# Kernel tuning notes

Measured on AMD Instinct MI355X. Metric: run time of the kernel, lower is better.

## Reference

```python
import jax, jax.numpy as jnp
import numpy as np

N_NODES = 100_000
NODES_PER_GRAPH = 100
NUM_GRAPHS = N_NODES // NODES_PER_GRAPH
N_EDGES = 1_600_000
NUM_FEATURES = 32
NUM_CLASSES = 10
K_POOL = 30          # DGCNN sort-pool k
OUT_LEN = 16
IN_LEN = 97          # 32+32+32+1 concatenated GCN features
NUM_ITER = 3


def setup_inputs() -> dict:
    key = jax.random.key(0)
    ks = jax.random.split(key, 12)
    x = jax.random.normal(ks[0], (N_NODES, NUM_FEATURES), dtype=jnp.float32)
    # edges constrained within each graph: gid*npg + local index
    gid = (jnp.arange(N_EDGES) % NUM_GRAPHS).astype(jnp.int64)
    src_loc = jax.random.randint(ks[1], (N_EDGES,), 0, NODES_PER_GRAPH)
    dst_loc = jax.random.randint(ks[2], (N_EDGES,), 0, NODES_PER_GRAPH)
    edge_src = gid * NODES_PER_GRAPH + src_loc
    edge_dst = gid * NODES_PER_GRAPH + dst_loc
    batch = jnp.arange(N_NODES, dtype=jnp.int64) // NODES_PER_GRAPH
    s = 1.0 / np.sqrt(NUM_FEATURES)
    params = dict(
        W1=jax.random.normal(ks[3], (NUM_FEATURES, 32), jnp.float32) * s,
        b1=jnp.zeros((32,), jnp.float32),
        W2=jax.random.normal(ks[4], (32, 32), jnp.float32) * (1/np.sqrt(32)),
        b2=jnp.zeros((32,), jnp.float32),
        W3=jax.random.normal(ks[5], (32, 32), jnp.float32) * (1/np.sqrt(32)),
        b3=jnp.zeros((32,), jnp.float32),
        W4=jax.random.normal(ks[6], (32, 1), jnp.float32) * (1/np.sqrt(32)),
        b4=jnp.zeros((1,), jnp.float32),
        Wcap=jax.random.normal(ks[7], (NUM_CLASSES, OUT_LEN, IN_LEN), jnp.float32) * (1/np.sqrt(IN_LEN)),
    )
    return dict(x=x, edge_src=edge_src, edge_dst=edge_dst, batch=batch, **params)


def gcn_conv(x, W, b, edge_src, edge_dst, dinv):
    # PyG GCNConv: h = xW, out[d] = sum_e dinv[s]*dinv[d]*h[s] (incl. self loops), + b
    h = x @ W
    msg = h[edge_src] * (dinv[edge_src] * dinv[edge_dst])[:, None]
    out = jax.ops.segment_sum(msg, edge_dst, num_segments=x.shape[0])
    out = out + h * (dinv * dinv)[:, None]  # self-loop term
    return out + b


def reference(x, edge_src, edge_dst, batch, W1, b1, W2, b2, W3, b3, W4, b4, Wcap):
    n = x.shape[0]
    # symmetric normalization with self loops (degree over incoming edges + 1)
    deg = jnp.zeros((n,), x.dtype).at[edge_dst].add(1.0) + 1.0
    dinv = jax.lax.rsqrt(deg)

    x1 = jnp.tanh(gcn_conv(x,  W1, b1, edge_src, edge_dst, dinv))
    x2 = jnp.tanh(gcn_conv(x1, W2, b2, edge_src, edge_dst, dinv))
    x3 = jnp.tanh(gcn_conv(x2, W3, b3, edge_src, edge_dst, dinv))
    x4 = jnp.tanh(gcn_conv(x3, W4, b4, edge_src, edge_dst, dinv))
    feat = jnp.concatenate([x1, x2, x3, x4], axis=-1)  # [N, 97]

    # global_sort_pool: per-graph descending sort on last channel, keep top-k nodes
    B = n // NODES_PER_GRAPH
    fg = feat.reshape(B, NODES_PER_GRAPH, IN_LEN)
    order = jnp.argsort(-fg[..., -1], axis=1)[:, :K_POOL]            # [B, k]
    pooled = jnp.take_along_axis(fg, order[..., None], axis=1)        # [B, k, 97]

    # CapsuleLinear, shared weight, k-means routing, Tanimoto similarity
    priors = jnp.einsum('bil,cel->bice', pooled, Wcap)                # [B, k, C, 16]
    pr_sq = jnp.sum(priors * priors, axis=-1)                         # [B, k, C]
    out = jnp.mean(priors, axis=1, keepdims=True)                     # [B, 1, C, 16]
    for _ in range(NUM_ITER):
        xy = jnp.sum(priors * out, axis=-1)                           # [B, k, C]
        out_sq = jnp.sum(out * out, axis=-1)                          # [B, 1, C]
        sim = xy / (pr_sq + out_sq - xy)                              # Tanimoto
        probs = jax.nn.softmax(sim, axis=1)[..., None]                # over in_capsules
        out = jnp.sum(probs * priors, axis=1, keepdims=True)
    out = out[:, 0]                                                   # [B, C, 16]
    classes = jnp.linalg.norm(out, axis=-1)                           # [B, C]
    return classes
```

## Files before the change

### kernel.cpp

```cpp
#include <hip/hip_runtime.h>
#include <math.h>

#define NGRAPH 1000
#define NPG    100
#define EPG    1600
#define NF     32
#define NC     10
#define KP     30
#define OUTL   16
#define INL    97
#define NITER  3

#define NTV    512
#define NTF    1024

#define XSTR   36
#define FSTR   100
#define HSTR   36
#define PSTR   164
#define CSRMAX 1920
#define ZROW   (NPG * XSTR)

#define WS_EDGES_BYTES ((size_t)NGRAPH * EPG * 4)
#define WCAPB_UINT4    2560
#define WS_V10_BYTES   (WS_EDGES_BYTES + (size_t)WCAPB_UINT4 * 16)

#define PIDX(i, c) ((i) * PSTR + (c) * OUTL)

typedef __attribute__((ext_vector_type(8))) short bf16x8;
typedef __attribute__((ext_vector_type(4))) float f32x4;

__device__ __forceinline__ float4 ld4(const float* p) { return *reinterpret_cast<const float4*>(p); }
__device__ __forceinline__ void st4(float* p, float4 v) { *reinterpret_cast<float4*>(p) = v; }
__device__ __forceinline__ float dot4(float4 a, float4 b) { return a.x*b.x + a.y*b.y + a.z*b.z + a.w*b.w; }
__device__ __forceinline__ float tanh_fast(float x) {
  float e = __expf(2.f * x);
  return 1.f - 2.f / (e + 1.f);
}
__device__ __forceinline__ unsigned f2bf(float f) {
  unsigned u = __float_as_uint(f);
  u += 0x7FFFu + ((u >> 16) & 1u);
  return u >> 16;
}

__global__ void prek_edges(const int* __restrict__ esrc, const int* __restrict__ edst,
                           unsigned int* __restrict__ wsE) {
  __shared__ unsigned int t[64][65];
  const int kb = blockIdx.x % (EPG / 64);
  const int gb = blockIdx.x / (EPG / 64);
  const int lane = threadIdx.x & 63;
  const int row  = threadIdx.x >> 6;
  #pragma unroll
  for (int r = row; r < 64; r += 4) {
    int k = kb * 64 + r;
    int g = gb * 64 + lane;
    if (g < NGRAPH) {
      int idx = k * NGRAPH + g;
      int si = esrc[idx] - g * NPG;
      int di = edst[idx] - g * NPG;
      t[r][lane] = (unsigned int)((si << 8) | di);
    }
  }
  __syncthreads();
  #pragma unroll
  for (int r = row; r < 64; r += 4) {
    int g = gb * 64 + r;
    int k = kb * 64 + lane;
    if (g < NGRAPH) wsE[(size_t)g * EPG + k] = t[lane][r];
  }
}

__global__ void prek_capB(const float* __restrict__ Wcap, uint4* __restrict__ wcapB) {
  int o = blockIdx.x * 256 + threadIdx.x;
  if (o >= WCAPB_UINT4) return;
  int ks  = o / 640;
  int rem = o - ks * 640;
  int n   = rem >> 6;
  int ln  = rem & 63;
  int e   = ln & 15;
  int k0  = ks * 32 + ((ln >> 4) << 3);
  const float* wr = Wcap + (n * OUTL + e) * INL;
  unsigned v[8];
  #pragma unroll
  for (int j = 0; j < 8; ++j) {
    int k = k0 + j;
    v[j] = f2bf((k < INL) ? wr[k] : 0.f);
  }
  uint4 pk;
  pk.x = v[0] | (v[1] << 16); pk.y = v[2] | (v[3] << 16);
  pk.z = v[4] | (v[5] << 16); pk.w = v[6] | (v[7] << 16);
  wcapB[o] = pk;
}

struct SMemV13 {
  float feat[NPG * FSTR];
  union {
    struct {
      float hs[(NPG + 1) * XSTR];
      float W[NF * NF];
      float bias2[2][NF];
      unsigned short csr16[CSRMAX];
      int cnt[NPG];
      float dinv[NPG];
      int ptr[NPG + 1];
    } a;
    struct {
      float priors[KP * PSTR];
      float prsq[KP * NC];
      float simbuf[KP * NC];
      float outv[NC * OUTL];
      uint4 pooledB[512];
    } b;
  } u;
  int order[KP];
};

__global__ __launch_bounds__(NTV, 4) void gcn_caps_v13(
    const float* __restrict__ x,
    const unsigned int* __restrict__ wsE,
    const float* __restrict__ W1, const float* __restrict__ b1,
    const float* __restrict__ W2, const float* __restrict__ b2,
    const float* __restrict__ W3, const float* __restrict__ b3,
    const float* __restrict__ W4, const float* __restrict__ b4,
    const uint4* __restrict__ wcapB,
    float* __restrict__ out)
{
  extern __shared__ char smraw[];
  SMemV13& s = *reinterpret_cast<SMemV13*>(smraw);
  const int g = blockIdx.x;
  const int tid = threadIdx.x;

  if (tid < NPG) s.u.a.cnt[tid] = 0;
  if (tid >= 128 && tid < 128 + XSTR) s.u.a.hs[ZROW + (tid - 128)] = 0.f;
  for (int i = tid; i < NF * NF; i += NTV) s.u.a.W[i] = W1[i];
  if (tid < NF) s.u.a.bias2[0][tid] = b1[tid];
  __syncthreads();

  const unsigned int* eg = wsE + (size_t)g * EPG;
  for (int k = tid; k < EPG; k += NTV) atomicAdd(&s.u.a.cnt[eg[k] & 0xFF], 1);
  __syncthreads();

  if (tid < 64) {
    int j = tid;
    int n0 = 2 * j, n1 = 2 * j + 1;
    int r0 = (n0 < NPG) ? s.u.a.cnt[n0] : 0;
    int r1 = (n1 < NPG) ? s.u.a.cnt[n1] : 0;
    int q0 = (r0 + 3) & ~3, q1 = (r1 + 3) & ~3;
    int t = q0 + q1;
    int run = t;
    #pragma unroll
    for (int off = 1; off < 64; off <<= 1) {
      int u = __shfl_up(run, off);
      if (j >= off) run += u;
    }
    int excl = run - t;
    if (n0 < NPG) {
      s.u.a.ptr[n0] = excl;
      s.u.a.dinv[n0] = rsqrtf((float)r0 + 1.0f);
      s.u.a.cnt[n0] = excl;
      for (int k = excl + r0; k < excl + q0; ++k) s.u.a.csr16[k] = (unsigned short)ZROW;
    }
    if (n1 < NPG) {
      int e1 = excl + q0;
      s.u.a.ptr[n1] = e1;
      s.u.a.dinv[n1] = rsqrtf((float)r1 + 1.0f);
      s.u.a.cnt[n1] = e1;
      for (int k = e1 + r1; k < e1 + q1; ++k) s.u.a.csr16[k] = (unsigned short)ZROW;
    }
    if (j == 63) s.u.a.ptr[NPG] = run;
  }
  __syncthreads();

  for (int k = tid; k < EPG; k += NTV) {
    unsigned int p = eg[k];
    int pos = atomicAdd(&s.u.a.cnt[p & 0xFF], 1);
    s.u.a.csr16[pos] = (unsigned short)(((p >> 8) & 0xFF) * XSTR);
  }
  __syncthreads();

  const float4* xr = reinterpret_cast<const float4*>(x + (size_t)g * NPG * NF);

  for (int l = 0; l < 3; ++l) {
    if (tid < 25 * 8) {
      int nd = tid >> 3, cq = tid & 7;
      float4 ac0 = make_float4(0,0,0,0), ac1 = ac0, ac2 = ac0, ac3 = ac0;
      #pragma unroll
      for (int kq = 0; kq < 8; ++kq) {
        float4 a0, a1, a2, a3;
        if (l == 0) {
          a0 = xr[(nd     ) * 8 + kq]; a1 = xr[(nd + 25) * 8 + kq];
          a2 = xr[(nd + 50) * 8 + kq]; a3 = xr[(nd + 75) * 8 + kq];
        } else {
          int cb = (l - 1) * NF + kq * 4;
          a0 = ld4(&s.feat[(nd     ) * FSTR + cb]);
          a1 = ld4(&s.feat[(nd + 25) * FSTR + cb]);
          a2 = ld4(&s.feat[(nd + 50) * FSTR + cb]);
          a3 = ld4(&s.feat[(nd + 75) * FSTR + cb]);
        }
        const float v0[4] = {a0.x, a0.y, a0.z, a0.w};
        const float v1[4] = {a1.x, a1.y, a1.z, a1.w};
        const float v2[4] = {a2.x, a2.y, a2.z, a2.w};
        const float v3[4] = {a3.x, a3.y, a3.z, a3.w};
        #pragma unroll
        for (int j = 0; j < 4; ++j) {
          float4 w4 = ld4(&s.u.a.W[(kq * 4 + j) * NF + cq * 4]);
          ac0.x += v0[j]*w4.x; ac0.y += v0[j]*w4.y; ac0.z += v0[j]*w4.z; ac0.w += v0[j]*w4.w;
          ac1.x += v1[j]*w4.x; ac1.y += v1[j]*w4.y; ac1.z += v1[j]*w4.z; ac1.w += v1[j]*w4.w;
          ac2.x += v2[j]*w4.x; ac2.y += v2[j]*w4.y; ac2.z += v2[j]*w4.z; ac2.w += v2[j]*w4.w;
          ac3.x += v3[j]*w4.x; ac3.y += v3[j]*w4.y; ac3.z += v3[j]*w4.z; ac3.w += v3[j]*w4.w;
        }
      }
      float d0 = s.u.a.dinv[nd], d1 = s.u.a.dinv[nd + 25];
      float d2 = s.u.a.dinv[nd + 50], d3 = s.u.a.dinv[nd + 75];
      ac0.x*=d0; ac0.y*=d0; ac0.z*=d0; ac0.w*=d0;
      ac1.x*=d1; ac1.y*=d1; ac1.z*=d1; ac1.w*=d1;
      ac2.x*=d2; ac2.y*=d2; ac2.z*=d2; ac2.w*=d2;
      ac3.x*=d3; ac3.y*=d3; ac3.z*=d3; ac3.w*=d3;
      st4(&s.u.a.hs[(nd     ) * XSTR + cq * 4], ac0);
      st4(&s.u.a.hs[(nd + 25) * XSTR + cq * 4], ac1);
      st4(&s.u.a.hs[(nd + 50) * XSTR + cq * 4], ac2);
      st4(&s.u.a.hs[(nd + 75) * XSTR + cq * 4], ac3);
    }
    __syncthreads();

    if (l == 0) {
      for (int i = tid; i < NF * NF; i += NTV) s.u.a.W[i] = W2[i];
      if (tid < NF) s.u.a.bias2[1][tid] = b2[tid];
    } else if (l == 1) {
      for (int i = tid; i < NF * NF; i += NTV) s.u.a.W[i] = W3[i];
      if (tid < NF) s.u.a.bias2[0][tid] = b3[tid];
    } else {
      if (tid < NF) s.u.a.W[tid] = W4[tid];
      if (tid == NTV - 1) s.u.a.bias2[1][0] = b4[0];
    }

    for (int o = tid; o < NPG * 16; o += NTV) {
      int d = o >> 4, fq4 = (o & 7) * 4, h = (o >> 3) & 1;
      int p0 = s.u.a.ptr[d], p1 = s.u.a.ptr[d + 1];
      float4 r = (h == 0) ? ld4(&s.u.a.hs[d * XSTR + fq4])
                          : make_float4(0.f, 0.f, 0.f, 0.f);
      for (int idx = p0 + h * 4; idx < p1; idx += 8) {
        uint2 c2 = *reinterpret_cast<const uint2*>(&s.u.a.csr16[idx]);
        int o0 = c2.x & 0xFFFF, o1 = c2.x >> 16;
        int o2 = c2.y & 0xFFFF, o3 = c2.y >> 16;
        float4 h0 = ld4(&s.u.a.hs[o0 + fq4]);
        float4 h1 = ld4(&s.u.a.hs[o1 + fq4]);
        float4 h2 = ld4(&s.u.a.hs[o2 + fq4]);
        float4 h3 = ld4(&s.u.a.hs[o3 + fq4]);
        r.x += (h0.x + h1.x) + (h2.x + h3.x);
        r.y += (h0.y + h1.y) + (h2.y + h3.y);
        r.z += (h0.z + h1.z) + (h2.z + h3.z);
        r.w += (h0.w + h1.w) + (h2.w + h3.w);
      }
      r.x += __shfl_xor(r.x, 8);
      r.y += __shfl_xor(r.y, 8);
      r.z += __shfl_xor(r.z, 8);
      r.w += __shfl_xor(r.w, 8);
      if (h == 0) {
        const float* bc = s.u.a.bias2[l & 1];
        float4 bq = ld4(&bc[fq4]);
        float di = s.u.a.dinv[d];
        float4 oo;
        oo.x = tanh_fast(di * r.x + bq.x);
        oo.y = tanh_fast(di * r.y + bq.y);
        oo.z = tanh_fast(di * r.z + bq.z);
        oo.w = tanh_fast(di * r.w + bq.w);
        st4(&s.feat[d * FSTR + l * NF + fq4], oo);
      }
    }
    __syncthreads();
  }

  if (tid < NPG) {
    float a = 0.f;
    #pragma unroll
    for (int kq = 0; kq < 8; ++kq)
      a += dot4(ld4(&s.feat[tid * FSTR + 2 * NF + kq * 4]), ld4(&s.u.a.W[kq * 4]));
    s.u.a.hs[tid * XSTR] = a * s.u.a.dinv[tid];
  }
  __syncthreads();
  for (int o = tid; o < NPG * 8; o += NTV) {
    int d = o >> 3, p = o & 7;
    int p0 = s.u.a.ptr[d], p1 = s.u.a.ptr[d + 1];
    float r = (p == 0) ? s.u.a.hs[d * XSTR] : 0.f;
    for (int idx = p0 + p; idx < p1; idx += 8) r += s.u.a.hs[s.u.a.csr16[idx]];
    r += __shfl_xor(r, 1);
    r += __shfl_xor(r, 2);
    r += __shfl_xor(r, 4);
    if (p == 0)
      s.feat[d * FSTR + 96] = tanh_fast(s.u.a.dinv[d] * r + s.u.a.bias2[1][0]);
  }
  __syncthreads();

  if (tid < NPG * 4) {
    int i = tid >> 2, p = tid & 3;
    float vv = s.feat[i * FSTR + 96];
    int j0 = p * 25, j1 = j0 + 25;
    int rank = 0;
    for (int j = j0; j < j1; ++j) {
      float vj = s.feat[j * FSTR + 96];
      rank += (vj > vv) || (vj == vv && j < i);
    }
    rank += __shfl_xor(rank, 1);
    rank += __shfl_xor(rank, 2);
    if (p == 0 && rank < KP) s.order[rank] = i;
  }
  __syncthreads();

  {
    int mt = tid >> 8, ks = (tid >> 6) & 3, ln = tid & 63;
    int i = mt * 16 + (ln & 15);
    int k0 = ks * 32 + ((ln >> 4) << 3);
    uint4 pk = make_uint4(0, 0, 0, 0);
    if (i < KP) {
      int row = s.order[i] * FSTR;
      float f[8];
      if (ks < 3) {
        float4 x0 = ld4(&s.feat[row + k0]);
        float4 x1 = ld4(&s.feat[row + k0 + 4]);
        f[0]=x0.x; f[1]=x0.y; f[2]=x0.z; f[3]=x0.w;
        f[4]=x1.x; f[5]=x1.y; f[6]=x1.z; f[7]=x1.w;
      } else {
        #pragma unroll
        for (int j = 0; j < 8; ++j) f[j] = 0.f;
        if (k0 == 96) f[0] = s.feat[row + 96];
      }
      pk.x = f2bf(f[0]) | (f2bf(f[1]) << 16);
      pk.y = f2bf(f[2]) | (f2bf(f[3]) << 16);
      pk.z = f2bf(f[4]) | (f2bf(f[5]) << 16);
      pk.w = f2bf(f[6]) | (f2bf(f[7]) << 16);
    }
    s.u.b.pooledB[(mt * 4 + ks) * 64 + ln] = pk;
  }
  __syncthreads();

  if (tid < 5 * 64) {
    int w = tid >> 6, ln = tid & 63;
    #pragma unroll
    for (int mt = 0; mt < 2; ++mt) {
      bf16x8 afr[4];
      #pragma unroll
      for (int ks = 0; ks < 4; ++ks) {
        uint4 raw = s.u.b.pooledB[(mt * 4 + ks) * 64 + ln];
        afr[ks] = __builtin_bit_cast(bf16x8, raw);
      }
      #pragma unroll
      for (int nn = 0; nn < 2; ++nn) {
        int n = w * 2 + nn;
        f32x4 acc = {0.f, 0.f, 0.f, 0.f};
        #pragma unroll
        for (int ks = 0; ks < 4; ++ks) {
          uint4 braw = wcapB[(ks * 10 + n) * 64 + ln];
          bf16x8 bfr = __builtin_bit_cast(bf16x8, braw);
          acc = __builtin_amdgcn_mfma_f32_16x16x32_bf16(afr[ks], bfr, acc, 0, 0, 0);
        }
        int ibase = mt * 16 + ((ln >> 4) << 2);
        int e = ln & 15;
        #pragma unroll
        for (int j = 0; j < 4; ++j) {
          int i = ibase + j;
          if (i < KP) s.u.b.priors[PIDX(i, n) + e] = acc[j];
        }
      }
    }
  }
  __syncthreads();

  if (tid < KP * NC) {
    int i = tid / NC, c = tid % NC;
    const float* pr = &s.u.b.priors[PIDX(i, c)];
    float a = 0.f;
    #pragma unroll
    for (int eq = 0; eq < 4; ++eq) { float4 p = ld4(pr + eq * 4); a += dot4(p, p); }
    s.u.b.prsq[tid] = a;
  }
  if (tid < NC * OUTL) {
    int c = tid >> 4, e = tid & 15;
    float a = 0.f;
    #pragma unroll
    for (int i = 0; i < KP; ++i) a += s.u.b.priors[PIDX(i, c) + e];
    s.u.b.outv[tid] = a * (1.0f / KP);
  }
  __syncthreads();

  for (int it = 0; it < NITER; ++it) {
    if (tid < KP * NC) {
      int i = tid / NC, c = tid % NC;
      const float* pr = &s.u.b.priors[PIDX(i, c)];
      const float* ov = &s.u.b.outv[c * OUTL];
      float xy = 0.f, oq = 0.f;
      #pragma unroll
      for (int eq = 0; eq < 4; ++eq) {
        float4 p = ld4(pr + eq * 4);
        float4 o = ld4(ov + eq * 4);
        xy += dot4(p, o); oq += dot4(o, o);
      }
      s.u.b.simbuf[tid] = xy / (s.u.b.prsq[tid] + oq - xy);
    }
    __syncthreads();
    if (tid < NC * OUTL) {
      int c = tid >> 4, e = tid & 15;
      float m = -1e30f;
      #pragma unroll
      for (int i = 0; i < KP; ++i) m = fmaxf(m, s.u.b.simbuf[i * NC + c]);
      float ss = 0.f, a = 0.f;
      #pragma unroll
      for (int i = 0; i < KP; ++i) {
        float w = __expf(s.u.b.simbuf[i * NC + c] - m);
        ss += w;
        a += w * s.u.b.priors[PIDX(i, c) + e];
      }
      s.u.b.outv[tid] = a / ss;
    }
    __syncthreads();
  }

  if (tid < NC) {
    const float* ov = &s.u.b.outv[tid * OUTL];
    float a = 0.f;
    #pragma unroll
    for (int eq = 0; eq < 4; ++eq) { float4 o = ld4(ov + eq * 4); a += dot4(o, o); }
    out[(size_t)g * NC + tid] = sqrtf(a);
  }
}

struct SMemF {
  float feat[NPG * FSTR];
  union {
    unsigned short epack[EPG];
    float priors[KP * PSTR];
  } u;
  union {
    float hs[NPG * HSTR];
    struct {
      float prsq[KP * NC];
      float simbuf[KP * NC];
      float outv[NC * OUTL];
      float smax[NC];
      float ssum[NC];
      int   order[KP];
    } r;
  } v;
  float W[NF * NF];
  float bias2[2][NF];
  unsigned char csr[EPG];
  int ptr[NPG + 1];
  int cnt[NPG];
  float dinv[NPG];
};

__global__ __launch_bounds__(NTF, 8) void gcn_caps_fused(
    const float* __restrict__ x,
    const int* __restrict__ esrc, const int* __restrict__ edst,
    const float* __restrict__ W1, const float* __restrict__ b1,
    const float* __restrict__ W2, const float* __restrict__ b2,
    const float* __restrict__ W3, const float* __restrict__ b3,
    const float* __restrict__ W4, const float* __restrict__ b4,
    const float* __restrict__ Wcap,
    float* __restrict__ out)
{
  extern __shared__ char smem_raw[];
  SMemF& s = *reinterpret_cast<SMemF*>(smem_raw);
  const int g = blockIdx.x;
  const int tid = threadIdx.x;

  if (tid < NPG) s.cnt[tid] = 0;
  for (int i = tid; i < NF * NF; i += NTF) s.W[i] = W1[i];
  if (tid < NF) s.bias2[0][tid] = b1[tid];
  __syncthreads();

  for (int k = tid; k < EPG; k += NTF) {
    int si = esrc[g + k * NGRAPH] - g * NPG;
    int di = edst[g + k * NGRAPH] - g * NPG;
    s.u.epack[k] = (unsigned short)((si << 8) | di);
    atomicAdd(&s.cnt[di], 1);
  }
  __syncthreads();

  if (tid < 64) {
    int j = tid;
    int a0 = (2 * j < NPG) ? s.cnt[2 * j] : 0;
    int a1 = (2 * j + 1 < NPG) ? s.cnt[2 * j + 1] : 0;
    int t = a0 + a1;
    int run = t;
    #pragma unroll
    for (int off = 1; off < 64; off <<= 1) {
      int u = __shfl_up(run, off);
      if (j >= off) run += u;
    }
    int excl = run - t;
    if (2 * j < NPG) s.ptr[2 * j] = excl;
    if (2 * j + 1 < NPG) s.ptr[2 * j + 1] = excl + a0;
    if (j == 63) s.ptr[NPG] = run;
  }
  __syncthreads();
  if (tid < NPG) {
    s.dinv[tid] = rsqrtf((float)s.cnt[tid] + 1.0f);
    s.cnt[tid] = s.ptr[tid];
  }
  __syncthreads();

  for (int k = tid; k < EPG; k += NTF) {
    int pk = s.u.epack[k];
    int pos = atomicAdd(&s.cnt[pk & 0xFF], 1);
    s.csr[pos] = (unsigned char)(pk >> 8);
  }
  __syncthreads();

  const float4* xr = reinterpret_cast<const float4*>(x + (size_t)g * NPG * NF);
  for (int l = 0; l < 3; ++l) {
    if (tid < NPG * 8) {
      int node = tid >> 3, cq = tid & 7;
      float4 acc = make_float4(0.f, 0.f, 0.f, 0.f);
      #pragma unroll
      for (int kq = 0; kq < 8; ++kq) {
        float4 a4 = (l == 0) ? xr[node * 8 + kq]
                             : ld4(&s.feat[node * FSTR + (l - 1) * NF + kq * 4]);
        const float av[4] = {a4.x, a4.y, a4.z, a4.w};
        #pragma unroll
        for (int j = 0; j < 4; ++j) {
          float4 w4 = ld4(&s.W[(kq * 4 + j) * NF + cq * 4]);
          acc.x += av[j] * w4.x; acc.y += av[j] * w4.y;
          acc.z += av[j] * w4.z; acc.w += av[j] * w4.w;
        }
      }
      float di = s.dinv[node];
      acc.x *= di; acc.y *= di; acc.z *= di; acc.w *= di;
      st4(&s.v.hs[node * HSTR + ((cq ^ (node >> 3)) & 7) * 4], acc);
    }
    __syncthreads();

    if (l == 0) {
      for (int i = tid; i < NF * NF; i += NTF) s.W[i] = W2[i];
      if (tid < NF) s.bias2[1][tid] = b2[tid];
    } else if (l == 1) {
      for (int i = tid; i < NF * NF; i += NTF) s.W[i] = W3[i];
      if (tid < NF) s.bias2[0][tid] = b3[tid];
    } else {
      if (tid < NF) s.W[tid] = W4[tid];
      if (tid == NTF - 1) s.bias2[1][0] = b4[0];
    }

    if (tid < NPG * 8) {
      int d = tid >> 3, fq = tid & 7;
      const float* bc = s.bias2[l & 1];
      float4 b4q = ld4(&bc[fq * 4]);
      float4 r = ld4(&s.v.hs[d * HSTR + ((fq ^ (d >> 3)) & 7) * 4]);
      int p0 = s.ptr[d], p1 = s.ptr[d + 1];
      int idx = p0;
      for (; idx + 1 < p1; idx += 2) {
        int sc0 = s.csr[idx], sc1 = s.csr[idx + 1];
        float4 h0 = ld4(&s.v.hs[sc0 * HSTR + ((fq ^ (sc0 >> 3)) & 7) * 4]);
        float4 h1 = ld4(&s.v.hs[sc1 * HSTR + ((fq ^ (sc1 >> 3)) & 7) * 4]);
        r.x += h0.x + h1.x; r.y += h0.y + h1.y;
        r.z += h0.z + h1.z; r.w += h0.w + h1.w;
      }
      if (idx < p1) {
        int sc = s.csr[idx];
        float4 hq = ld4(&s.v.hs[sc * HSTR + ((fq ^ (sc >> 3)) & 7) * 4]);
        r.x += hq.x; r.y += hq.y; r.z += hq.z; r.w += hq.w;
      }
      float di = s.dinv[d];
      float4 o;
      o.x = tanh_fast(di * r.x + b4q.x);
      o.y = tanh_fast(di * r.y + b4q.y);
      o.z = tanh_fast(di * r.z + b4q.z);
      o.w = tanh_fast(di * r.w + b4q.w);
      st4(&s.feat[d * FSTR + l * NF + fq * 4], o);
    }
    __syncthreads();
  }

  float* hsf = s.v.hs;
  if (tid < NPG) {
    float a = 0.f;
    #pragma unroll
    for (int kq = 0; kq < 8; ++kq)
      a += dot4(ld4(&s.feat[tid * FSTR + 64 + kq * 4]), ld4(&s.W[kq * 4]));
    hsf[tid] = a * s.dinv[tid];
  }
  __syncthreads();
  if (tid < NPG) {
    float r = hsf[tid];
    int p0 = s.ptr[tid], p1 = s.ptr[tid + 1];
    for (int idx = p0; idx < p1; ++idx) r += hsf[s.csr[idx]];
    s.feat[tid * FSTR + 96] = tanh_fast(s.dinv[tid] * r + s.bias2[1][0]);
  }
  __syncthreads();

  if (tid < NPG * 8) {
    int i = tid >> 3, p = tid & 7;
    float vv = s.feat[i * FSTR + 96];
    int j0 = p * 13, j1 = min(NPG, j0 + 13);
    int rank = 0;
    for (int j = j0; j < j1; ++j) {
      float vj = s.feat[j * FSTR + 96];
      rank += (vj > vv) || (vj == vv && j < i);
    }
    rank += __shfl_xor(rank, 1);
    rank += __shfl_xor(rank, 2);
    rank += __shfl_xor(rank, 4);
    if (p == 0 && rank < KP) s.v.r.order[rank] = i;
  }
  __syncthreads();

  if (tid < KP * OUTL) {
    int i = tid >> 4, e = tid & 15;
    int row = s.v.r.order[i] * FSTR;
    float acc[NC];
    #pragma unroll
    for (int c = 0; c < NC; ++c) acc[c] = 0.f;
    for (int c = 0; c < NC; ++c) {
      float a = 0.f;
      for (int l = 0; l < INL; ++l) a += s.feat[row + l] * Wcap[(c * OUTL + e) * INL + l];
      acc[c] = a;
    }
    #pragma unroll
    for (int c = 0; c < NC; ++c) s.u.priors[PIDX(i, c) + e] = acc[c];
  }
  __syncthreads();

  if (tid < KP * NC) {
    int i = tid / NC, c = tid % NC;
    const float* pr = &s.u.priors[PIDX(i, c)];
    float a = 0.f;
    #pragma unroll
    for (int eq = 0; eq < 4; ++eq) { float4 p = ld4(pr + eq * 4); a += dot4(p, p); }
    s.v.r.prsq[tid] = a;
  }
  if (tid < NC * OUTL) {
    int c = tid >> 4, e = tid & 15;
    float a = 0.f;
    #pragma unroll
    for (int i = 0; i < KP; ++i) a += s.u.priors[PIDX(i, c) + e];
    s.v.r.outv[tid] = a * (1.0f / KP);
  }
  __syncthreads();

  for (int it = 0; it < NITER; ++it) {
    if (tid < KP * NC) {
      int i = tid / NC, c = tid % NC;
      const float* pr = &s.u.priors[PIDX(i, c)];
      const float* ov = &s.v.r.outv[c * OUTL];
      float xy = 0.f, oq = 0.f;
      #pragma unroll
      for (int eq = 0; eq < 4; ++eq) {
        float4 p = ld4(pr + eq * 4);
        float4 o = ld4(ov + eq * 4);
        xy += dot4(p, o); oq += dot4(o, o);
      }
      s.v.r.simbuf[tid] = xy / (s.v.r.prsq[tid] + oq - xy);
    }
    __syncthreads();
    if (tid < NC) {
      float m = -1e30f;
      #pragma unroll
      for (int i = 0; i < KP; ++i) m = fmaxf(m, s.v.r.simbuf[i * NC + tid]);
      float ss = 0.f;
      #pragma unroll
      for (int i = 0; i < KP; ++i) ss += __expf(s.v.r.simbuf[i * NC + tid] - m);
      s.v.r.smax[tid] = m;
      s.v.r.ssum[tid] = 1.f / ss;
    }
    __syncthreads();
    if (tid < NC * OUTL) {
      int c = tid >> 4, e = tid & 15;
      float m = s.v.r.smax[c], is = s.v.r.ssum[c], a = 0.f;
      #pragma unroll
      for (int i = 0; i < KP; ++i)
        a += __expf(s.v.r.simbuf[i * NC + c] - m) * s.u.priors[PIDX(i, c) + e];
      s.v.r.outv[tid] = a * is;
    }
    __syncthreads();
  }

  if (tid < NC) {
    const float* ov = &s.v.r.outv[tid * OUTL];
    float a = 0.f;
    #pragma unroll
    for (int eq = 0; eq < 4; ++eq) { float4 o = ld4(ov + eq * 4); a += dot4(o, o); }
    out[(size_t)g * NC + tid] = sqrtf(a);
  }
}

extern "C" void kernel_launch(void* const* d_in, const int* in_sizes, int n_in,
                              void* d_out, int out_size, void* d_ws, size_t ws_size,
                              hipStream_t stream) {
  const float* x    = (const float*)d_in[0];
  const int*   esrc = (const int*)d_in[1];
  const int*   edst = (const int*)d_in[2];
  const float* W1 = (const float*)d_in[4];
  const float* b1 = (const float*)d_in[5];
  const float* W2 = (const float*)d_in[6];
  const float* b2 = (const float*)d_in[7];
  const float* W3 = (const float*)d_in[8];
  const float* b3 = (const float*)d_in[9];
  const float* W4 = (const float*)d_in[10];
  const float* b4 = (const float*)d_in[11];
  const float* Wcap = (const float*)d_in[12];
  float* outp = (float*)d_out;

  if (ws_size >= WS_V10_BYTES) {
    unsigned int* wsE = (unsigned int*)d_ws;
    uint4* wcapB = (uint4*)((char*)d_ws + WS_EDGES_BYTES);
    (void)hipFuncSetAttribute((const void*)gcn_caps_v13,
                              hipFuncAttributeMaxDynamicSharedMemorySize, (int)sizeof(SMemV13));
    prek_edges<<<(EPG / 64) * 16, 256, 0, stream>>>(esrc, edst, wsE);
    prek_capB<<<(WCAPB_UINT4 + 255) / 256, 256, 0, stream>>>(Wcap, wcapB);
    gcn_caps_v13<<<NGRAPH, NTV, sizeof(SMemV13), stream>>>(
        x, wsE, W1, b1, W2, b2, W3, b3, W4, b4, wcapB, outp);
  } else {
    (void)hipFuncSetAttribute((const void*)gcn_caps_fused,
                              hipFuncAttributeMaxDynamicSharedMemorySize, (int)sizeof(SMemF));
    gcn_caps_fused<<<NGRAPH, NTF, sizeof(SMemF), stream>>>(
        x, esrc, edst, W1, b1, W2, b2, W3, b3, W4, b4, Wcap, outp);
  }
}
```

Measured before the change: 81.37 us.

## Process two graphs per 1024-thread block with shared weights

Each block now handles two graphs with 1024 threads instead of one graph with 512, so the grid halves. Per-graph shared buffers are duplicated while the GCN weights and biases move out of the union and are shared between both graphs, which halves weight staging per graph and fills more lanes in the small per-graph phases. The final 32-to-1 GCN projection is also reworked to spread each node over 8 lanes with shuffle reductions. In exchange, LDS per block roughly doubles and launch_bounds(1024,4) may not be achievable, which could cut residency or force register spills.

```diff
diff --git a/kernel.cpp b/kernel.cpp
--- a/kernel.cpp
+++ b/kernel.cpp
@@ -11,7 +11,7 @@
 #define INL    97
 #define NITER  3
 
-#define NTV    512
+#define NTV    1024
 #define NTF    1024
 
 #define XSTR   36
@@ -92,30 +92,30 @@
   wcapB[o] = pk;
 }
 
-struct SMemV13 {
-  float feat[NPG * FSTR];
+struct SMemV14 {
+  float feat[2][NPG * FSTR];
   union {
     struct {
-      float hs[(NPG + 1) * XSTR];
-      float W[NF * NF];
-      float bias2[2][NF];
-      unsigned short csr16[CSRMAX];
-      int cnt[NPG];
-      float dinv[NPG];
-      int ptr[NPG + 1];
+      float hs[2][(NPG + 1) * XSTR];
+      unsigned short csr16[2][CSRMAX];
+      int cnt[2][NPG];
+      float dinv[2][NPG];
+      int ptr[2][NPG + 1];
     } a;
     struct {
-      float priors[KP * PSTR];
-      float prsq[KP * NC];
-      float simbuf[KP * NC];
-      float outv[NC * OUTL];
-      uint4 pooledB[512];
+      float priors[2][KP * PSTR];
+      float prsq[2][KP * NC];
+      float simbuf[2][KP * NC];
+      float outv[2][NC * OUTL];
+      uint4 pooledB[2][512];
     } b;
   } u;
-  int order[KP];
+  float W[NF * NF];
+  float bias2[2][NF];
+  int order[2][KP];
 };
 
-__global__ __launch_bounds__(NTV, 4) void gcn_caps_v13(
+__global__ __launch_bounds__(NTV, 4) void gcn_caps_v14(
     const float* __restrict__ x,
     const unsigned int* __restrict__ wsE,
     const float* __restrict__ W1, const float* __restrict__ b1,
@@ -126,25 +126,41 @@
     float* __restrict__ out)
 {
   extern __shared__ char smraw[];
-  SMemV13& s = *reinterpret_cast<SMemV13*>(smraw);
-  const int g = blockIdx.x;
+  SMemV14& s = *reinterpret_cast<SMemV14*>(smraw);
+  const int g0 = blockIdx.x * 2;
   const int tid = threadIdx.x;
 
-  if (tid < NPG) s.u.a.cnt[tid] = 0;
-  if (tid >= 128 && tid < 128 + XSTR) s.u.a.hs[ZROW + (tid - 128)] = 0.f;
-  for (int i = tid; i < NF * NF; i += NTV) s.u.a.W[i] = W1[i];
-  if (tid < NF) s.u.a.bias2[0][tid] = b1[tid];
-  __syncthreads();
-
-  const unsigned int* eg = wsE + (size_t)g * EPG;
-  for (int k = tid; k < EPG; k += NTV) atomicAdd(&s.u.a.cnt[eg[k] & 0xFF], 1);
-  __syncthreads();
-
-  if (tid < 64) {
-    int j = tid;
+  const unsigned int* eg0 = wsE + (size_t)g0 * EPG;
+  const unsigned int* eg1 = wsE + (size_t)(g0 + 1) * EPG;
+  const float4* xr0 = reinterpret_cast<const float4*>(x + (size_t)g0 * NPG * NF);
+  const float4* xr1 = reinterpret_cast<const float4*>(x + (size_t)(g0 + 1) * NPG * NF);
+
+  if (tid < 2 * NPG) {
+    int gi = tid / NPG, i = tid - gi * NPG;
+    s.u.a.cnt[gi][i] = 0;
+  }
+  if (tid >= 256 && tid < 256 + 2 * XSTR) {
+    int t = tid - 256;
+    int gi = t / XSTR, i = t - gi * XSTR;
+    s.u.a.hs[gi][ZROW + i] = 0.f;
+  }
+  for (int i = tid; i < NF * NF; i += NTV) s.W[i] = W1[i];
+  if (tid >= 512 && tid < 512 + NF) s.bias2[0][tid - 512] = b1[tid - 512];
+  __syncthreads();
+
+  for (int k = tid; k < 2 * EPG; k += NTV) {
+    int gi = k >= EPG;
+    int kk = k - gi * EPG;
+    unsigned int p = (gi ? eg1 : eg0)[kk];
+    atomicAdd(&s.u.a.cnt[gi][p & 0xFF], 1);
+  }
+  __syncthreads();
+
+  if (tid < 128) {
+    int wv = tid >> 6, j = tid & 63;
     int n0 = 2 * j, n1 = 2 * j + 1;
-    int r0 = (n0 < NPG) ? s.u.a.cnt[n0] : 0;
-    int r1 = (n1 < NPG) ? s.u.a.cnt[n1] : 0;
+    int r0 = (n0 < NPG) ? s.u.a.cnt[wv][n0] : 0;
+    int r1 = (n1 < NPG) ? s.u.a.cnt[wv][n1] : 0;
     int q0 = (r0 + 3) & ~3, q1 = (r1 + 3) & ~3;
     int t = q0 + q1;
     int run = t;
@@ -155,47 +171,51 @@
     }
     int excl = run - t;
     if (n0 < NPG) {
-      s.u.a.ptr[n0] = excl;
-      s.u.a.dinv[n0] = rsqrtf((float)r0 + 1.0f);
-      s.u.a.cnt[n0] = excl;
-      for (int k = excl + r0; k < excl + q0; ++k) s.u.a.csr16[k] = (unsigned short)ZROW;
+      s.u.a.ptr[wv][n0] = excl;
+      s.u.a.dinv[wv][n0] = rsqrtf((float)r0 + 1.0f);
+      s.u.a.cnt[wv][n0] = excl;
+      for (int k = excl + r0; k < excl + q0; ++k) s.u.a.csr16[wv][k] = (unsigned short)ZROW;
     }
     if (n1 < NPG) {
       int e1 = excl + q0;
-      s.u.a.ptr[n1] = e1;
-      s.u.a.dinv[n1] = rsqrtf((float)r1 + 1.0f);
-      s.u.a.cnt[n1] = e1;
-      for (int k = e1 + r1; k < e1 + q1; ++k) s.u.a.csr16[k] = (unsigned short)ZROW;
-    }
-    if (j == 63) s.u.a.ptr[NPG] = run;
-  }
-  __syncthreads();
-
-  for (int k = tid; k < EPG; k += NTV) {
-    unsigned int p = eg[k];
-    int pos = atomicAdd(&s.u.a.cnt[p & 0xFF], 1);
-    s.u.a.csr16[pos] = (unsigned short)(((p >> 8) & 0xFF) * XSTR);
-  }
-  __syncthreads();
-
-  const float4* xr = reinterpret_cast<const float4*>(x + (size_t)g * NPG * NF);
+      s.u.a.ptr[wv][n1] = e1;
+      s.u.a.dinv[wv][n1] = rsqrtf((float)r1 + 1.0f);
+      s.u.a.cnt[wv][n1] = e1;
+      for (int k = e1 + r1; k < e1 + q1; ++k) s.u.a.csr16[wv][k] = (unsigned short)ZROW;
+    }
+    if (j == 63) s.u.a.ptr[wv][NPG] = run;
+  }
+  __syncthreads();
+
+  for (int k = tid; k < 2 * EPG; k += NTV) {
+    int gi = k >= EPG;
+    int kk = k - gi * EPG;
+    unsigned int p = (gi ? eg1 : eg0)[kk];
+    int pos = atomicAdd(&s.u.a.cnt[gi][p & 0xFF], 1);
+    s.u.a.csr16[gi][pos] = (unsigned short)(((p >> 8) & 0xFF) * XSTR);
+  }
+  __syncthreads();
 
   for (int l = 0; l < 3; ++l) {
-    if (tid < 25 * 8) {
-      int nd = tid >> 3, cq = tid & 7;
+    if (tid < 2 * 200) {
+      int gi = tid >= 200;
+      int t = tid - gi * 200;
+      int nd = t >> 3, cq = t & 7;
+      const float4* xp = gi ? xr1 : xr0;
+      const float* fp = s.feat[gi];
       float4 ac0 = make_float4(0,0,0,0), ac1 = ac0, ac2 = ac0, ac3 = ac0;
       #pragma unroll
       for (int kq = 0; kq < 8; ++kq) {
         float4 a0, a1, a2, a3;
         if (l == 0) {
-          a0 = xr[(nd     ) * 8 + kq]; a1 = xr[(nd + 25) * 8 + kq];
-          a2 = xr[(nd + 50) * 8 + kq]; a3 = xr[(nd + 75) * 8 + kq];
+          a0 = xp[(nd     ) * 8 + kq]; a1 = xp[(nd + 25) * 8 + kq];
+          a2 = xp[(nd + 50) * 8 + kq]; a3 = xp[(nd + 75) * 8 + kq];
         } else {
           int cb = (l - 1) * NF + kq * 4;
-          a0 = ld4(&s.feat[(nd     ) * FSTR + cb]);
-          a1 = ld4(&s.feat[(nd + 25) * FSTR + cb]);
-          a2 = ld4(&s.feat[(nd + 50) * FSTR + cb]);
-          a3 = ld4(&s.feat[(nd + 75) * FSTR + cb]);
+          a0 = ld4(&fp[(nd     ) * FSTR + cb]);
+          a1 = ld4(&fp[(nd + 25) * FSTR + cb]);
+          a2 = ld4(&fp[(nd + 50) * FSTR + cb]);
+          a3 = ld4(&fp[(nd + 75) * FSTR + cb]);
         }
         const float v0[4] = {a0.x, a0.y, a0.z, a0.w};
         const float v1[4] = {a1.x, a1.y, a1.z, a1.w};
@@ -203,50 +223,55 @@
         const float v3[4] = {a3.x, a3.y, a3.z, a3.w};
         #pragma unroll
         for (int j = 0; j < 4; ++j) {
-          float4 w4 = ld4(&s.u.a.W[(kq * 4 + j) * NF + cq * 4]);
+          float4 w4 = ld4(&s.W[(kq * 4 + j) * NF + cq * 4]);
           ac0.x += v0[j]*w4.x; ac0.y += v0[j]*w4.y; ac0.z += v0[j]*w4.z; ac0.w += v0[j]*w4.w;
           ac1.x += v1[j]*w4.x; ac1.y += v1[j]*w4.y; ac1.z += v1[j]*w4.z; ac1.w += v1[j]*w4.w;
           ac2.x += v2[j]*w4.x; ac2.y += v2[j]*w4.y; ac2.z += v2[j]*w4.z; ac2.w += v2[j]*w4.w;
           ac3.x += v3[j]*w4.x; ac3.y += v3[j]*w4.y; ac3.z += v3[j]*w4.z; ac3.w += v3[j]*w4.w;
         }
       }
-      float d0 = s.u.a.dinv[nd], d1 = s.u.a.dinv[nd + 25];
-      float d2 = s.u.a.dinv[nd + 50], d3 = s.u.a.dinv[nd + 75];
+      const float* dv = s.u.a.dinv[gi];
+      float d0 = dv[nd], d1 = dv[nd + 25], d2 = dv[nd + 50], d3 = dv[nd + 75];
       ac0.x*=d0; ac0.y*=d0; ac0.z*=d0; ac0.w*=d0;
       ac1.x*=d1; ac1.y*=d1; ac1.z*=d1; ac1.w*=d1;
       ac2.x*=d2; ac2.y*=d2; ac2.z*=d2; ac2.w*=d2;
       ac3.x*=d3; ac3.y*=d3; ac3.z*=d3; ac3.w*=d3;
-      st4(&s.u.a.hs[(nd     ) * XSTR + cq * 4], ac0);
-      st4(&s.u.a.hs[(nd + 25) * XSTR + cq * 4], ac1);
-      st4(&s.u.a.hs[(nd + 50) * XSTR + cq * 4], ac2);
-      st4(&s.u.a.hs[(nd + 75) * XSTR + cq * 4], ac3);
+      float* hp = s.u.a.hs[gi];
+      st4(&hp[(nd     ) * XSTR + cq * 4], ac0);
+      st4(&hp[(nd + 25) * XSTR + cq * 4], ac1);
+      st4(&hp[(nd + 50) * XSTR + cq * 4], ac2);
+      st4(&hp[(nd + 75) * XSTR + cq * 4], ac3);
     }
     __syncthreads();
 
     if (l == 0) {
-      for (int i = tid; i < NF * NF; i += NTV) s.u.a.W[i] = W2[i];
-      if (tid < NF) s.u.a.bias2[1][tid] = b2[tid];
+      for (int i = tid; i < NF * NF; i += NTV) s.W[i] = W2[i];
+      if (tid >= 512 && tid < 512 + NF) s.bias2[1][tid - 512] = b2[tid - 512];
     } else if (l == 1) {
-      for (int i = tid; i < NF * NF; i += NTV) s.u.a.W[i] = W3[i];
-      if (tid < NF) s.u.a.bias2[0][tid] = b3[tid];
+      for (int i = tid; i < NF * NF; i += NTV) s.W[i] = W3[i];
+      if (tid >= 512 && tid < 512 + NF) s.bias2[0][tid - 512] = b3[tid - 512];
     } else {
-      if (tid < NF) s.u.a.W[tid] = W4[tid];
-      if (tid == NTV - 1) s.u.a.bias2[1][0] = b4[0];
-    }
-
-    for (int o = tid; o < NPG * 16; o += NTV) {
-      int d = o >> 4, fq4 = (o & 7) * 4, h = (o >> 3) & 1;
-      int p0 = s.u.a.ptr[d], p1 = s.u.a.ptr[d + 1];
-      float4 r = (h == 0) ? ld4(&s.u.a.hs[d * XSTR + fq4])
+      if (tid >= 512 && tid < 512 + NF) s.W[tid - 512] = W4[tid - 512];
+      if (tid == NTV - 1) s.bias2[1][0] = b4[0];
+    }
+
+    for (int o = tid; o < 2 * NPG * 16; o += NTV) {
+      int gi = o >= NPG * 16;
+      int oo = o - gi * NPG * 16;
+      int d = oo >> 4, fq4 = (oo & 7) * 4, h = (oo >> 3) & 1;
+      const unsigned short* cs = s.u.a.csr16[gi];
+      const float* hp = s.u.a.hs[gi];
+      int p0 = s.u.a.ptr[gi][d], p1 = s.u.a.ptr[gi][d + 1];
+      float4 r = (h == 0) ? ld4(&hp[d * XSTR + fq4])
                           : make_float4(0.f, 0.f, 0.f, 0.f);
       for (int idx = p0 + h * 4; idx < p1; idx += 8) {
-        uint2 c2 = *reinterpret_cast<const uint2*>(&s.u.a.csr16[idx]);
+        uint2 c2 = *reinterpret_cast<const uint2*>(&cs[idx]);
         int o0 = c2.x & 0xFFFF, o1 = c2.x >> 16;
         int o2 = c2.y & 0xFFFF, o3 = c2.y >> 16;
-        float4 h0 = ld4(&s.u.a.hs[o0 + fq4]);
-        float4 h1 = ld4(&s.u.a.hs[o1 + fq4]);
-        float4 h2 = ld4(&s.u.a.hs[o2 + fq4]);
-        float4 h3 = ld4(&s.u.a.hs[o3 + fq4]);
+        float4 h0 = ld4(&hp[o0 + fq4]);
+        float4 h1 = ld4(&hp[o1 + fq4]);
+        float4 h2 = ld4(&hp[o2 + fq4]);
+        float4 h3 = ld4(&hp[o3 + fq4]);
         r.x += (h0.x + h1.x) + (h2.x + h3.x);
         r.y += (h0.y + h1.y) + (h2.y + h3.y);
         r.z += (h0.z + h1.z) + (h2.z + h3.z);
@@ -257,137 +282,162 @@
       r.z += __shfl_xor(r.z, 8);
       r.w += __shfl_xor(r.w, 8);
       if (h == 0) {
-        const float* bc = s.u.a.bias2[l & 1];
+        const float* bc = s.bias2[l & 1];
         float4 bq = ld4(&bc[fq4]);
-        float di = s.u.a.dinv[d];
-        float4 oo;
-        oo.x = tanh_fast(di * r.x + bq.x);
-        oo.y = tanh_fast(di * r.y + bq.y);
-        oo.z = tanh_fast(di * r.z + bq.z);
-        oo.w = tanh_fast(di * r.w + bq.w);
-        st4(&s.feat[d * FSTR + l * NF + fq4], oo);
-      }
-    }
-    __syncthreads();
-  }
-
-  if (tid < NPG) {
-    float a = 0.f;
-    #pragma unroll
-    for (int kq = 0; kq < 8; ++kq)
-      a += dot4(ld4(&s.feat[tid * FSTR + 2 * NF + kq * 4]), ld4(&s.u.a.W[kq * 4]));
-    s.u.a.hs[tid * XSTR] = a * s.u.a.dinv[tid];
-  }
-  __syncthreads();
-  for (int o = tid; o < NPG * 8; o += NTV) {
-    int d = o >> 3, p = o & 7;
-    int p0 = s.u.a.ptr[d], p1 = s.u.a.ptr[d + 1];
-    float r = (p == 0) ? s.u.a.hs[d * XSTR] : 0.f;
-    for (int idx = p0 + p; idx < p1; idx += 8) r += s.u.a.hs[s.u.a.csr16[idx]];
+        float di = s.u.a.dinv[gi][d];
+        float4 oo4;
+        oo4.x = tanh_fast(di * r.x + bq.x);
+        oo4.y = tanh_fast(di * r.y + bq.y);
+        oo4.z = tanh_fast(di * r.z + bq.z);
+        oo4.w = tanh_fast(di * r.w + bq.w);
+        st4(&s.feat[gi][d * FSTR + l * NF + fq4], oo4);
+      }
+    }
+    __syncthreads();
+  }
+
+  for (int o = tid; o < 2 * NPG * 8; o += NTV) {
+    int gi = o >= NPG * 8;
+    int oo = o - gi * NPG * 8;
+    int d = oo >> 3, fq4 = (oo & 7) * 4;
+    float r = dot4(ld4(&s.feat[gi][d * FSTR + 2 * NF + fq4]), ld4(&s.W[fq4]));
+    r += __shfl_xor(r, 1);
+    r += __shfl_xor(r, 2);
+    r += __shfl_xor(r, 4);
+    if ((oo & 7) == 0) s.u.a.hs[gi][d * XSTR] = r * s.u.a.dinv[gi][d];
+  }
+  __syncthreads();
+
+  for (int o = tid; o < 2 * NPG * 8; o += NTV) {
+    int gi = o >= NPG * 8;
+    int oo = o - gi * NPG * 8;
+    int d = oo >> 3, p = oo & 7;
+    const unsigned short* cs = s.u.a.csr16[gi];
+    const float* hp = s.u.a.hs[gi];
+    int p0 = s.u.a.ptr[gi][d], p1 = s.u.a.ptr[gi][d + 1];
+    float r = (p == 0) ? hp[d * XSTR] : 0.f;
+    for (int idx = p0 + p; idx < p1; idx += 8) r += hp[cs[idx]];
     r += __shfl_xor(r, 1);
     r += __shfl_xor(r, 2);
     r += __shfl_xor(r, 4);
     if (p == 0)
-      s.feat[d * FSTR + 96] = tanh_fast(s.u.a.dinv[d] * r + s.u.a.bias2[1][0]);
-  }
-  __syncthreads();
-
-  if (tid < NPG * 4) {
-    int i = tid >> 2, p = tid & 3;
-    float vv = s.feat[i * FSTR + 96];
+      s.feat[gi][d * FSTR + 96] = tanh_fast(s.u.a.dinv[gi][d] * r + s.bias2[1][0]);
+  }
+  __syncthreads();
+
+  if (tid < 2 * NPG * 4) {
+    int gi = tid >= NPG * 4;
+    int oo = tid - gi * NPG * 4;
+    int i = oo >> 2, p = oo & 3;
+    const float* fp = s.feat[gi];
+    float vv = fp[i * FSTR + 96];
     int j0 = p * 25, j1 = j0 + 25;
     int rank = 0;
     for (int j = j0; j < j1; ++j) {
-      float vj = s.feat[j * FSTR + 96];
+      float vj = fp[j * FSTR + 96];
       rank += (vj > vv) || (vj == vv && j < i);
     }
     rank += __shfl_xor(rank, 1);
     rank += __shfl_xor(rank, 2);
-    if (p == 0 && rank < KP) s.order[rank] = i;
+    if (p == 0 && rank < KP) s.order[gi][rank] = i;
   }
   __syncthreads();
 
   {
-    int mt = tid >> 8, ks = (tid >> 6) & 3, ln = tid & 63;
+    int gi = tid >= 512;
+    int t = tid - gi * 512;
+    int mt = t >> 8, ks = (t >> 6) & 3, ln = t & 63;
     int i = mt * 16 + (ln & 15);
     int k0 = ks * 32 + ((ln >> 4) << 3);
     uint4 pk = make_uint4(0, 0, 0, 0);
     if (i < KP) {
-      int row = s.order[i] * FSTR;
+      int row = s.order[gi][i] * FSTR;
+      const float* fp = s.feat[gi];
       float f[8];
       if (ks < 3) {
-        float4 x0 = ld4(&s.feat[row + k0]);
-        float4 x1 = ld4(&s.feat[row + k0 + 4]);
+        float4 x0 = ld4(&fp[row + k0]);
+        float4 x1 = ld4(&fp[row + k0 + 4]);
         f[0]=x0.x; f[1]=x0.y; f[2]=x0.z; f[3]=x0.w;
         f[4]=x1.x; f[5]=x1.y; f[6]=x1.z; f[7]=x1.w;
       } else {
         #pragma unroll
         for (int j = 0; j < 8; ++j) f[j] = 0.f;
-        if (k0 == 96) f[0] = s.feat[row + 96];
+        if (k0 == 96) f[0] = fp[row + 96];
       }
       pk.x = f2bf(f[0]) | (f2bf(f[1]) << 16);
       pk.y = f2bf(f[2]) | (f2bf(f[3]) << 16);
       pk.z = f2bf(f[4]) | (f2bf(f[5]) << 16);
       pk.w = f2bf(f[6]) | (f2bf(f[7]) << 16);
     }
-    s.u.b.pooledB[(mt * 4 + ks) * 64 + ln] = pk;
-  }
-  __syncthreads();
-
-  if (tid < 5 * 64) {
-    int w = tid >> 6, ln = tid & 63;
-    #pragma unroll
-    for (int mt = 0; mt < 2; ++mt) {
-      bf16x8 afr[4];
-      #pragma unroll
-      for (int ks = 0; ks < 4; ++ks) {
-        uint4 raw = s.u.b.pooledB[(mt * 4 + ks) * 64 + ln];
-        afr[ks] = __builtin_bit_cast(bf16x8, raw);
-      }
-      #pragma unroll
-      for (int nn = 0; nn < 2; ++nn) {
-        int n = w * 2 + nn;
-        f32x4 acc = {0.f, 0.f, 0.f, 0.f};
+    s.u.b.pooledB[gi][(mt * 4 + ks) * 64 + ln] = pk;
+  }
+  __syncthreads();
+
+  {
+    int w = tid >> 6;
+    if (w < 10) {
+      int gi = w >= 5;
+      int wv = w - gi * 5;
+      int ln = tid & 63;
+      float* pri = s.u.b.priors[gi];
+      const uint4* pb = s.u.b.pooledB[gi];
+      #pragma unroll
+      for (int mt = 0; mt < 2; ++mt) {
+        bf16x8 afr[4];
         #pragma unroll
-        for (int ks = 0; ks < 4; ++ks) {
-          uint4 braw = wcapB[(ks * 10 + n) * 64 + ln];
-          bf16x8 bfr = __builtin_bit_cast(bf16x8, braw);
-          acc = __builtin_amdgcn_mfma_f32_16x16x32_bf16(afr[ks], bfr, acc, 0, 0, 0);
+        for (int ks = 0; ks < 4; ++ks)
+          afr[ks] = __builtin_bit_cast(bf16x8, pb[(mt * 4 + ks) * 64 + ln]);
+        #pragma unroll
+        for (int nn = 0; nn < 2; ++nn) {
+          int n = wv * 2 + nn;
+          f32x4 acc = {0.f, 0.f, 0.f, 0.f};
+          #pragma unroll
+          for (int ks = 0; ks < 4; ++ks) {
+            bf16x8 bfr = __builtin_bit_cast(bf16x8, wcapB[(ks * 10 + n) * 64 + ln]);
+            acc = __builtin_amdgcn_mfma_f32_16x16x32_bf16(afr[ks], bfr, acc, 0, 0, 0);
+          }
+          int ibase = mt * 16 + ((ln >> 4) << 2);
+          int e = ln & 15;
+          #pragma unroll
+          for (int j = 0; j < 4; ++j) {
+            int i = ibase + j;
+            if (i < KP) pri[PIDX(i, n) + e] = acc[j];
+          }
         }
-        int ibase = mt * 16 + ((ln >> 4) << 2);
-        int e = ln & 15;
-        #pragma unroll
-        for (int j = 0; j < 4; ++j) {
-          int i = ibase + j;
-          if (i < KP) s.u.b.priors[PIDX(i, n) + e] = acc[j];
-        }
-      }
-    }
-  }
-  __syncthreads();
-
-  if (tid < KP * NC) {
-    int i = tid / NC, c = tid % NC;
-    const float* pr = &s.u.b.priors[PIDX(i, c)];
+      }
+    }
+  }
+  __syncthreads();
+
+  if (tid < 2 * KP * NC) {
+    int gi = tid >= KP * NC;
+    int t = tid - gi * KP * NC;
+    int i = t / NC, c = t % NC;
+    const float* pr = &s.u.b.priors[gi][PIDX(i, c)];
     float a = 0.f;
     #pragma unroll
     for (int eq = 0; eq < 4; ++eq) { float4 p = ld4(pr + eq * 4); a += dot4(p, p); }
-    s.u.b.prsq[tid] = a;
-  }
-  if (tid < NC * OUTL) {
-    int c = tid >> 4, e = tid & 15;
+    s.u.b.prsq[gi][t] = a;
+  }
+  if (tid < 2 * NC * OUTL) {
+    int gi = tid >= NC * OUTL;
+    int t = tid - gi * NC * OUTL;
+    int c = t >> 4, e = t & 15;
+    const float* pri = s.u.b.priors[gi];
     float a = 0.f;
     #pragma unroll
-    for (int i = 0; i < KP; ++i) a += s.u.b.priors[PIDX(i, c) + e];
-    s.u.b.outv[tid] = a * (1.0f / KP);
+    for (int i = 0; i < KP; ++i) a += pri[PIDX(i, c) + e];
+    s.u.b.outv[gi][t] = a * (1.0f / KP);
   }
   __syncthreads();
 
   for (int it = 0; it < NITER; ++it) {
-    if (tid < KP * NC) {
-      int i = tid / NC, c = tid % NC;
-      const float* pr = &s.u.b.priors[PIDX(i, c)];
-      const float* ov = &s.u.b.outv[c * OUTL];
+    if (tid < 2 * KP * NC) {
+      int gi = tid >= KP * NC;
+      int t = tid - gi * KP * NC;
+      int i = t / NC, c = t % NC;
+      const float* pr = &s.u.b.priors[gi][PIDX(i, c)];
+      const float* ov = &s.u.b.outv[gi][c * OUTL];
       float xy = 0.f, oq = 0.f;
       #pragma unroll
       for (int eq = 0; eq < 4; ++eq) {
@@ -395,32 +445,38 @@
         float4 o = ld4(ov + eq * 4);
         xy += dot4(p, o); oq += dot4(o, o);
       }
-      s.u.b.simbuf[tid] = xy / (s.u.b.prsq[tid] + oq - xy);
-    }
-    __syncthreads();
-    if (tid < NC * OUTL) {
-      int c = tid >> 4, e = tid & 15;
+      s.u.b.simbuf[gi][t] = xy / (s.u.b.prsq[gi][t] + oq - xy);
+    }
+    __syncthreads();
+    if (tid < 2 * NC * OUTL) {
+      int gi = tid >= NC * OUTL;
+      int t = tid - gi * NC * OUTL;
+      int c = t >> 4, e = t & 15;
+      const float* sb = s.u.b.simbuf[gi];
+      const float* pri = s.u.b.priors[gi];
       float m = -1e30f;
       #pragma unroll
-      for (int i = 0; i < KP; ++i) m = fmaxf(m, s.u.b.simbuf[i * NC + c]);
+      for (int i = 0; i < KP; ++i) m = fmaxf(m, sb[i * NC + c]);
       float ss = 0.f, a = 0.f;
       #pragma unroll
       for (int i = 0; i < KP; ++i) {
-        float w = __expf(s.u.b.simbuf[i * NC + c] - m);
+        float w = __expf(sb[i * NC + c] - m);
         ss += w;
-        a += w * s.u.b.priors[PIDX(i, c) + e];
-      }
-      s.u.b.outv[tid] = a / ss;
-    }
-    __syncthreads();
-  }
-
-  if (tid < NC) {
-    const float* ov = &s.u.b.outv[tid * OUTL];
+        a += w * pri[PIDX(i, c) + e];
+      }
+      s.u.b.outv[gi][t] = a / ss;
+    }
+    __syncthreads();
+  }
+
+  if (tid < 2 * NC) {
+    int gi = tid >= NC;
+    int c = tid - gi * NC;
+    const float* ov = &s.u.b.outv[gi][c * OUTL];
     float a = 0.f;
     #pragma unroll
     for (int eq = 0; eq < 4; ++eq) { float4 o = ld4(ov + eq * 4); a += dot4(o, o); }
-    out[(size_t)g * NC + tid] = sqrtf(a);
+    out[(size_t)(g0 + gi) * NC + c] = sqrtf(a);
   }
 }
 
@@ -703,11 +759,11 @@
   if (ws_size >= WS_V10_BYTES) {
     unsigned int* wsE = (unsigned int*)d_ws;
     uint4* wcapB = (uint4*)((char*)d_ws + WS_EDGES_BYTES);
-    (void)hipFuncSetAttribute((const void*)gcn_caps_v13,
-                              hipFuncAttributeMaxDynamicSharedMemorySize, (int)sizeof(SMemV13));
+    (void)hipFuncSetAttribute((const void*)gcn_caps_v14,
+                              hipFuncAttributeMaxDynamicSharedMemorySize, (int)sizeof(SMemV14));
     prek_edges<<<(EPG / 64) * 16, 256, 0, stream>>>(esrc, edst, wsE);
     prek_capB<<<(WCAPB_UINT4 + 255) / 256, 256, 0, stream>>>(Wcap, wcapB);
-    gcn_caps_v13<<<NGRAPH, NTV, sizeof(SMemV13), stream>>>(
+    gcn_caps_v14<<<NGRAPH / 2, NTV, sizeof(SMemV14), stream>>>(
         x, wsE, W1, b1, W2, b2, W3, b3, W4, b4, wcapB, outp);
   } else {
     (void)hipFuncSetAttribute((const void*)gcn_caps_fused,
```

After: 86.26 us. 6.0% more time.
